# Performance work log

Measured on AMD Instinct MI355X. Metric: run time of the kernel, lower is better.

Reference implementation:

```python
import jax, jax.numpy as jnp
import numpy as np

K = 20
EPS = 1e-5   # BatchNorm eps (eval mode: running_mean=0, running_var=1)
SLOPE = 0.2


def knn_idx(x, k):
    # x: [B,F,N] -> idx [B,N,k]; top-k of negative squared distance (includes self)
    xx = jnp.sum(x * x, axis=1)                       # [B,N]
    inner = jnp.einsum('bfn,bfm->bnm', x, x)          # [B,N,N]
    neg_d = 2.0 * inner - xx[:, :, None] - xx[:, None, :]
    _, idx = jax.lax.top_k(neg_d, k)
    return idx


def gather_neighbors(x_nt, idx):
    # x_nt [B,N,F], idx [B,N,k] -> [B,N,k,F]
    return jax.vmap(lambda xt, ix: xt[ix])(x_nt, idx)


def group_layer(x_bfn, idx):
    # GroupLayer: [B,F,N] -> [B,2F,N,k] = cat(neigh - center, neigh)
    x_nt = jnp.transpose(x_bfn, (0, 2, 1))
    neigh = gather_neighbors(x_nt, idx)
    feat = jnp.concatenate([neigh - x_nt[:, :, None, :], neigh], axis=-1)
    return jnp.transpose(feat, (0, 3, 1, 2))


def eigen_graph(pts_bfn, k):
    # pts_bfn [B,3,N] -> feature [B,15,N], idx_EU [B,N,k], idx_EI [B,N,k]
    B, _, N = pts_bfn.shape
    idx_eu = knn_idx(pts_bfn, k)
    pts_nt = jnp.transpose(pts_bfn, (0, 2, 1))        # [B,N,3]
    neigh = gather_neighbors(pts_nt, idx_eu)          # [B,N,k,3]
    diff = neigh - pts_nt[:, :, None, :]
    cov = jnp.einsum('bnki,bnkj->bnij', diff, diff)   # [B,N,3,3] symmetric PSD
    eigval, eigvec = jnp.linalg.eigh(cov)             # [B,N,3], [B,N,3,3]
    feature = jnp.concatenate([pts_nt, eigval, eigvec.reshape(B, N, 9)], axis=2)
    idx_ei = knn_idx(jnp.transpose(eigval, (0, 2, 1)), k)
    return jnp.transpose(feature, (0, 2, 1)), idx_eu, idx_ei


def first_group_layer(x_bfn, idx_eu, idx_ei):
    # x_bfn [B,15,N]: [:,0:3]=xyz, [:,3:6]=eigenvalues -> [B,12,N,k]
    xyz = jnp.transpose(x_bfn[:, 0:3, :], (0, 2, 1))
    eig = jnp.transpose(x_bfn[:, 3:6, :], (0, 2, 1))
    nx = gather_neighbors(xyz, idx_eu)
    gx = jnp.concatenate([nx - xyz[:, :, None, :], nx], axis=-1)
    ne = gather_neighbors(eig, idx_ei)
    ge = jnp.concatenate([ne - eig[:, :, None, :], ne], axis=-1)
    out = jnp.concatenate([gx, ge], axis=-1)
    return jnp.transpose(out, (0, 3, 1, 2))


def graph_distance(pts_bfn, idx):
    pts_nt = jnp.transpose(pts_bfn, (0, 2, 1))
    d = gather_neighbors(pts_nt, idx) - pts_nt[:, :, None, :]
    s = jnp.sum(d * d, axis=-1)
    return jnp.sqrt(jnp.maximum(s, 1e-12))[:, None, :, :]  # [B,1,N,k]


def conv_bn_lrelu(x, w, g, b):
    # 1x1 conv (no bias) + eval-mode BN + LeakyReLU(0.2)
    if x.ndim == 4:
        y = jnp.einsum('oc,bcnk->bonk', w, x)
        g_, b_ = g[None, :, None, None], b[None, :, None, None]
    else:
        y = jnp.einsum('oc,bcn->bon', w, x)
        g_, b_ = g[None, :, None], b[None, :, None]
    y = y / jnp.sqrt(1.0 + EPS) * g_ + b_
    return jax.nn.leaky_relu(y, SLOPE)


def fps(points, n_samples):
    # furthest point sampling, start at index 0. points [B,N,3] -> [B,S] int32
    B, N, _ = points.shape
    init = jnp.zeros((B,), jnp.int32)
    dist0 = jnp.full((B, N), 1e10, points.dtype)

    def body(carry, _):
        dist, last = carry
        lastp = jnp.take_along_axis(points, last[:, None, None].astype(jnp.int32), axis=1)
        d = jnp.sum((points - lastp) ** 2, axis=-1)
        dist = jnp.minimum(dist, d)
        nxt = jnp.argmax(dist, axis=-1).astype(jnp.int32)
        return (dist, nxt), nxt

    (_, _), rest = jax.lax.scan(body, (dist0, init), None, length=n_samples - 1)
    return jnp.concatenate([init[None, :], rest], axis=0).T


def gather_op(x_bcn, idx):
    # x [B,C,N], idx [B,S] -> [B,C,S]
    return jnp.take_along_axis(x_bcn, idx[:, None, :], axis=2)


def forward(x, conv1_w, bn1_g, bn1_b, conv2_w, bn2_g, bn2_b, conv3_w, bn3_g, bn3_b,
            conv5_w, bn5_g, bn5_b, lin1_w, bn6_g, bn6_b, lin2_w, lin2_b,
            bn7_g, bn7_b, lin3_w, lin3_b):
    B, _, N1 = x.shape
    N2, N3 = N1 // 2, N1 // 4
    pts1 = jnp.transpose(x, (0, 2, 1))  # [B,N,3]

    # GSCM layer 1 (first layer)
    feat, idx_eu, idx_ei = eigen_graph(x, K)
    g = first_group_layer(feat, idx_eu, idx_ei)            # [B,12,N1,K]
    g = jnp.concatenate([g, graph_distance(x, idx_eu)], axis=1)  # [B,13,N1,K]
    x1 = conv_bn_lrelu(g, conv1_w, bn1_g, bn1_b).max(axis=-1)     # [B,64,N1]

    # downsample to N2
    id2 = fps(pts1, N2)
    pts2_bfn = gather_op(x, id2)                            # [B,3,N2]
    x1_ds = gather_op(x1, id2)                              # [B,64,N2]

    # GSCM layer 2
    _, idx_eu2, idx_ei2 = eigen_graph(pts2_bfn, K)
    g2 = jnp.concatenate([group_layer(x1_ds, idx_eu2), group_layer(x1_ds, idx_ei2)], axis=1)
    x2 = conv_bn_lrelu(g2, conv2_w, bn2_g, bn2_b).max(axis=-1)    # [B,64,N2]

    # downsample to N3
    pts2_nt = jnp.transpose(pts2_bfn, (0, 2, 1))
    id3 = fps(pts2_nt, N3)
    pts3_bfn = gather_op(pts2_bfn, id3)
    x2_ds = gather_op(x2, id3)
    x1_ds = gather_op(x1_ds, id3)

    # GSCM layer 3
    _, idx_eu3, idx_ei3 = eigen_graph(pts3_bfn, K)
    g3 = jnp.concatenate([group_layer(x2_ds, idx_eu3), group_layer(x2_ds, idx_ei3)], axis=1)
    x3 = conv_bn_lrelu(g3, conv3_w, bn3_g, bn3_b).max(axis=-1)    # [B,128,N3]

    h = jnp.concatenate([x1_ds, x2_ds, x3], axis=1)        # [B,256,N3]
    h = conv_bn_lrelu(h, conv5_w, bn5_g, bn5_b)            # [B,emb,N3]
    h = jnp.concatenate([h.max(axis=-1), h.mean(axis=-1)], axis=1)  # [B,2*emb]

    y = jnp.einsum('oi,bi->bo', lin1_w, h)
    y = jax.nn.leaky_relu(y / jnp.sqrt(1.0 + EPS) * bn6_g + bn6_b, SLOPE)
    y = jnp.einsum('oi,bi->bo', lin2_w, y) + lin2_b
    y = jax.nn.leaky_relu(y / jnp.sqrt(1.0 + EPS) * bn7_g + bn7_b, SLOPE)
    return jnp.einsum('oi,bi->bo', lin3_w, y) + lin3_b     # [B,40]


def setup_inputs() -> dict:
    key = jax.random.key(0)
    ks = jax.random.split(key, 10)
    B, N, EMB, OUT = 16, 1024, 1024, 40

    def w(k_, o, i):
        return jax.random.normal(k_, (o, i), jnp.float32) * (1.0 / np.sqrt(i))

    return {
        'x': jax.random.normal(ks[0], (B, 3, N), jnp.float32),
        'conv1_w': w(ks[1], 64, 13), 'bn1_g': jnp.ones((64,)), 'bn1_b': jnp.zeros((64,)),
        'conv2_w': w(ks[2], 64, 256), 'bn2_g': jnp.ones((64,)), 'bn2_b': jnp.zeros((64,)),
        'conv3_w': w(ks[3], 128, 256), 'bn3_g': jnp.ones((128,)), 'bn3_b': jnp.zeros((128,)),
        'conv5_w': w(ks[4], EMB, 256), 'bn5_g': jnp.ones((EMB,)), 'bn5_b': jnp.zeros((EMB,)),
        'lin1_w': w(ks[5], 512, 2 * EMB), 'bn6_g': jnp.ones((512,)), 'bn6_b': jnp.zeros((512,)),
        'lin2_w': w(ks[6], 256, 512), 'lin2_b': jnp.zeros((256,)),
        'bn7_g': jnp.ones((256,)), 'bn7_b': jnp.zeros((256,)),
        'lin3_w': w(ks[7], OUT, 256), 'lin3_b': jnp.zeros((OUT,)),
    }


def reference(x, conv1_w, bn1_g, bn1_b, conv2_w, bn2_g, bn2_b, conv3_w, bn3_g, bn3_b,
              conv5_w, bn5_g, bn5_b, lin1_w, bn6_g, bn6_b, lin2_w, lin2_b,
              bn7_g, bn7_b, lin3_w, lin3_b):
    return forward(x, conv1_w, bn1_g, bn1_b, conv2_w, bn2_g, bn2_b, conv3_w, bn3_g, bn3_b,
                   conv5_w, bn5_g, bn5_b, lin1_w, bn6_g, bn6_b, lin2_w, lin2_b,
                   bn7_g, bn7_b, lin3_w, lin3_b)
```

## Files before the change

kernel.cpp:

```cpp
#include <hip/hip_runtime.h>
#include <math.h>

#define KNB 20
constexpr float BN_INV = 0.9999950000374997f;
constexpr float SLOPE = 0.2f;

__device__ __forceinline__ float lrelu(float v){ return v >= 0.f ? v : SLOPE*v; }

__global__ __launch_bounds__(256) void prep_kernel(const float* __restrict__ x, float* __restrict__ pts,
                            const float* __restrict__ conv2w, float* __restrict__ Wc2,
                            const float* __restrict__ conv3w, float* __restrict__ Wc3){
  int i = blockIdx.x*256 + threadIdx.x;
  if (i < 16*1024){
    int b = i >> 10, n = i & 1023;
    const float* xb = x + (size_t)b*3*1024;
    float* p = pts + (size_t)i*3;
    p[0]=xb[n]; p[1]=xb[1024+n]; p[2]=xb[2048+n];
  } else if (i < 16*1024 + 64*64){
    int e = i - 16*1024;
    int o = e >> 6, c = e & 63;
    float wa=conv2w[(size_t)o*256+c], wb=conv2w[(size_t)o*256+64+c];
    float wc=conv2w[(size_t)o*256+128+c], wd=conv2w[(size_t)o*256+192+c];
    Wc2[((size_t)0*64+o)*64+c]=wa+wb; Wc2[((size_t)1*64+o)*64+c]=wc+wd; Wc2[((size_t)2*64+o)*64+c]=wa+wc;
  } else if (i < 16*1024 + 64*64 + 128*64){
    int e = i - 16*1024 - 64*64;
    int o = e >> 6, c = e & 63;
    float wa=conv3w[(size_t)o*256+c], wb=conv3w[(size_t)o*256+64+c];
    float wc=conv3w[(size_t)o*256+128+c], wd=conv3w[(size_t)o*256+192+c];
    Wc3[((size_t)0*128+o)*64+c]=wa+wb; Wc3[((size_t)1*128+o)*64+c]=wc+wd; Wc3[((size_t)2*128+o)*64+c]=wa+wc;
  }
}

template<int N, bool TOGLOBAL>
__device__ void knn_core(const float* __restrict__ pts, int* __restrict__ idx_global,
                         int* __restrict__ sOut, int chunk, int b, float4* sp){
#pragma clang fp contract(off)
  constexpr int E = N/64;
  int t = threadIdx.x;
  const float* pb = pts + (size_t)b*N*3;
  for (int e = t; e < N; e += 256){
    float x0=pb[e*3], x1=pb[e*3+1], x2=pb[e*3+2];
    sp[e] = make_float4(x0, x1, x2, (x0*x0 + x1*x1) + x2*x2);
  }
  __syncthreads();
  int wave = t >> 6, lane = t & 63;
  int row = chunk*4 + wave;
  float4 P = sp[row];
  float nd[E];
  #pragma unroll
  for (int i=0;i<E;++i){
    float4 Q = sp[lane + i*64];
    float inner = (P.x*Q.x + P.y*Q.y) + P.z*Q.z;
    nd[i] = (2.0f*inner - P.w) - Q.w;
  }
  int myout = 0;
  for (int j=0;j<KNB;++j){
    float bv = nd[0]; int bi = lane;
    #pragma unroll
    for (int i=1;i<E;++i){
      if (nd[i] > bv){ bv = nd[i]; bi = lane + i*64; }
    }
    #pragma unroll
    for (int off=1; off<64; off<<=1){
      float ov = __shfl_xor(bv, off);
      int oi = __shfl_xor(bi, off);
      if (ov > bv || (ov == bv && oi < bi)){ bv = ov; bi = oi; }
    }
    if (lane == j) myout = bi;
    if (lane == (bi & 63)){
      int slot = bi >> 6;
      #pragma unroll
      for (int i=0;i<E;++i) if (i == slot) nd[i] = -INFINITY;
    }
  }
  if (TOGLOBAL){
    if (lane < KNB) idx_global[((size_t)b*N + row)*KNB + lane] = myout;
  } else {
    if (lane < KNB) sOut[lane] = myout;
  }
}

template<int N>
__global__ __launch_bounds__(256) void knn_kernel(const float* __restrict__ pts, int* __restrict__ idx){
  __shared__ float4 sp[N];
  knn_core<N,true>(pts, idx, nullptr, blockIdx.x, blockIdx.y, sp);
}

#define DECLQ(i) float4 Q##i = sp[(i)*64+lane]; float D##i = 1e10f; \
  asm volatile("" : "+v"(Q##i.x), "+v"(Q##i.y), "+v"(Q##i.z));
#define UPD(i, B) { float dx=Q##i.x-L.x; float dy=Q##i.y-L.y; float dz=Q##i.z-L.z; \
  float dd=fminf(D##i,(dx*dx+dy*dy)+dz*dz); D##i=dd; \
  unsigned long long k=((unsigned long long)__float_as_uint(dd)<<32)|(unsigned long long)(nl-(unsigned)((i)*64)); \
  if(k>B)B=k; }
#define DPPMAX(ctrl) { unsigned lo=(unsigned)bk, hi=(unsigned)(bk>>32); \
  unsigned lo2=(unsigned)__builtin_amdgcn_mov_dpp((int)lo, ctrl, 0xF, 0xF, true); \
  unsigned hi2=(unsigned)__builtin_amdgcn_mov_dpp((int)hi, ctrl, 0xF, 0xF, true); \
  unsigned long long ok=((unsigned long long)hi2<<32)|lo2; if(ok>bk)bk=ok; }
#define FPS_TAIL \
      unsigned long long kl_ = b0>b1?b0:b1; unsigned long long kh_ = b2>b3?b2:b3; \
      unsigned long long bk = kl_>kh_?kl_:kh_; \
      DPPMAX(0xB1) DPPMAX(0x4E) DPPMAX(0x124) DPPMAX(0x128) \
      { unsigned long long ok=__shfl_xor(bk,16); if(ok>bk)bk=ok; } \
      { unsigned long long ok=__shfl_xor(bk,32); if(ok>bk)bk=ok; } \
      last = (int)(~(unsigned int)bk); \
      if (lane==0) idout[(size_t)b*M + s] = last;

template<int N, int M>
__device__ void fps_body(const float* __restrict__ pts, int* __restrict__ idout,
                         int b, float4* sp){
#pragma clang fp contract(off)
  constexpr int E = N/64;
  int tid = threadIdx.x;
  const float* pb = pts + (size_t)b*N*3;
  for (int e=tid; e<N; e+=256){
    sp[e] = make_float4(pb[e*3], pb[e*3+1], pb[e*3+2], 0.f);
  }
  __syncthreads();
  if (tid >= 64) return;
  __builtin_amdgcn_s_setprio(1);
  int lane = tid;
  unsigned int nl = ~(unsigned int)lane;
  int last = 0;
  if (lane==0) idout[(size_t)b*M] = 0;
  if constexpr (E == 16){
    DECLQ(0) DECLQ(1) DECLQ(2) DECLQ(3) DECLQ(4) DECLQ(5) DECLQ(6) DECLQ(7)
    DECLQ(8) DECLQ(9) DECLQ(10) DECLQ(11) DECLQ(12) DECLQ(13) DECLQ(14) DECLQ(15)
    for (int s=1; s<M; ++s){
      float4 L = sp[last];
      unsigned long long b0=0ULL,b1=0ULL,b2=0ULL,b3=0ULL;
      UPD(0,b0) UPD(1,b1) UPD(2,b2) UPD(3,b3)
      UPD(4,b0) UPD(5,b1) UPD(6,b2) UPD(7,b3)
      UPD(8,b0) UPD(9,b1) UPD(10,b2) UPD(11,b3)
      UPD(12,b0) UPD(13,b1) UPD(14,b2) UPD(15,b3)
      FPS_TAIL
    }
  } else {
    DECLQ(0) DECLQ(1) DECLQ(2) DECLQ(3) DECLQ(4) DECLQ(5) DECLQ(6) DECLQ(7)
    for (int s=1; s<M; ++s){
      float4 L = sp[last];
      unsigned long long b0=0ULL,b1=0ULL,b2=0ULL,b3=0ULL;
      UPD(0,b0) UPD(1,b1) UPD(2,b2) UPD(3,b3)
      UPD(4,b0) UPD(5,b1) UPD(6,b2) UPD(7,b3)
      FPS_TAIL
    }
  }
}

template<int N, int M>
__global__ __launch_bounds__(256, 1) void mega_knn_fps_kernel(const float* __restrict__ pts,
    int* __restrict__ knn_idx, int* __restrict__ fps_id){
  __shared__ float4 sp[N];
  if (blockIdx.x < 16){
    fps_body<N,M>(pts, fps_id, blockIdx.x, sp);
  } else {
    int bx = blockIdx.x - 16;
    knn_core<N,true>(pts, knn_idx, nullptr, bx % (N/4), bx / (N/4), sp);
  }
}

template<int N>
__global__ void cov_eig_kernel(const float* __restrict__ pts, const int* __restrict__ idx,
                               float* __restrict__ eigval){
  int i = blockIdx.x*blockDim.x + threadIdx.x;
  if (i >= 16*N) return;
  int b = i / N, n = i % N;
  const float* pb = pts + (size_t)b*N*3;
  const int* ix = idx + (size_t)i*KNB;
  float cx = pb[n*3], cy = pb[n*3+1], cz = pb[n*3+2];
  float c00=0,c01=0,c02=0,c11=0,c12=0,c22=0;
  for (int k=0;k<KNB;++k){
    int m = ix[k];
    float dx = pb[m*3]-cx, dy = pb[m*3+1]-cy, dz = pb[m*3+2]-cz;
    c00 += dx*dx; c01 += dx*dy; c02 += dx*dz;
    c11 += dy*dy; c12 += dy*dz; c22 += dz*dz;
  }
  double a00=c00,a01=c01,a02=c02,a11=c11,a12=c12,a22=c22;
  double p1 = a01*a01 + a02*a02 + a12*a12;
  double q = (a00+a11+a22)/3.0;
  double b00=a00-q, b11=a11-q, b22=a22-q;
  double p2 = b00*b00+b11*b11+b22*b22 + 2.0*p1;
  double e0,e1,e2;
  if (p2 <= 0.0){
    e0=e1=e2=q;
  } else {
    double p = sqrt(p2/6.0);
    double det = b00*(b11*b22 - a12*a12) - a01*(a01*b22 - a12*a02) + a02*(a01*a12 - b11*a02);
    double r = det / (2.0*p*p*p);
    r = fmin(1.0, fmax(-1.0, r));
    double phi = acos(r)/3.0;
    double big = q + 2.0*p*cos(phi);
    double sml = q + 2.0*p*cos(phi + 2.0943951023931953);
    double mid = 3.0*q - big - sml;
    e0 = sml; e1 = mid; e2 = big;
  }
  float* ev = eigval + (size_t)i*3;
  ev[0]=(float)e0; ev[1]=(float)e1; ev[2]=(float)e2;
}

__global__ __launch_bounds__(256) void knn_ei_stage1_kernel(
    const float* __restrict__ eig, const float* __restrict__ pts,
    const int* __restrict__ idx_eu,
    const float* __restrict__ w, const float* __restrict__ g, const float* __restrict__ bb,
    float* __restrict__ x1){
  constexpr int N = 1024;
  __shared__ float4 sp[N];
  __shared__ int sIei[4][KNB];
  __shared__ float feat[4][13][KNB];
  int b = blockIdx.y, chunk = blockIdx.x;
  int t = threadIdx.x, wave = t>>6, lane = t&63;
  knn_core<N,false>(eig, nullptr, &sIei[wave][0], chunk, b, sp);
  int row = chunk*4 + wave;
  size_t i = (size_t)b*N + row;
  const float* pb = pts + (size_t)b*N*3;
  if (lane < KNB){
    int ieu = idx_eu[i*KNB + lane];
    int iei = sIei[wave][lane];
    float4 ne4 = sp[iei];
    float4 ee4 = sp[row];
    float d2 = 0.f;
    #pragma unroll
    for (int f=0; f<3; ++f){
      float nx = pb[ieu*3+f], xx = pb[row*3+f];
      float dfv = nx - xx;
      feat[wave][f][lane] = dfv; feat[wave][3+f][lane] = nx;
      float ne = (f==0)? ne4.x : ((f==1)? ne4.y : ne4.z);
      float ee = (f==0)? ee4.x : ((f==1)? ee4.y : ee4.z);
      feat[wave][6+f][lane] = ne - ee; feat[wave][9+f][lane] = ne;
      d2 += dfv*dfv;
    }
    feat[wave][12][lane] = sqrtf(fmaxf(d2, 1e-12f));
  }
  __syncthreads();
  float wr[13];
  #pragma unroll
  for (int c=0;c<13;++c) wr[c] = w[lane*13+c];
  float sg = BN_INV * g[lane], sb = bb[lane];
  float mx = -INFINITY;
  for (int k=0;k<KNB;++k){
    float s = 0.f;
    #pragma unroll
    for (int c=0;c<13;++c) s = fmaf(wr[c], feat[wave][c][k], s);
    mx = fmaxf(mx, lrelu(fmaf(s, sg, sb)));
  }
  x1[i*64 + lane] = mx;
}

template<int COUT, int N>
__device__ void gm_body(const float* __restrict__ eig,
    const float* __restrict__ PQR, int Mtot,
    const int* __restrict__ idx_eu,
    const float* __restrict__ g, const float* __restrict__ bb,
    float* __restrict__ xout, int chunk, int b, float4* sp, int* sIeiW){
  int t = threadIdx.x, wave = t>>6, lane = t&63;
  knn_core<N,false>(eig, nullptr, sIeiW, chunk, b, sp);
  __syncthreads();
  int row = chunk*4 + wave;
  size_t i = (size_t)b*N + row;
  const float* P = PQR;
  const float* Q = PQR + (size_t)Mtot*COUT;
  const float* R = PQR + (size_t)2*Mtot*COUT;
  for (int o = lane; o < COUT; o += 64){
    float base = R[i*COUT + o];
    float sg = BN_INV*g[o], sb = bb[o];
    float mx = -INFINITY;
    for (int k=0;k<KNB;++k){
      int eu = idx_eu[i*KNB + k];
      int ei = sIeiW[k];
      float v = P[((size_t)b*N + eu)*COUT + o] + Q[((size_t)b*N + ei)*COUT + o] - base;
      mx = fmaxf(mx, lrelu(fmaf(v, sg, sb)));
    }
    xout[i*COUT + o] = mx;
  }
}

template<int COUT, int N>
__global__ __launch_bounds__(256) void knn_ei_gm_kernel(
    const float* __restrict__ eig, const float* __restrict__ PQR, int Mtot,
    const int* __restrict__ idx_eu, const float* __restrict__ g, const float* __restrict__ bb,
    float* __restrict__ xout){
  __shared__ float4 sp[N];
  __shared__ int sIei[4][KNB];
  int wave = threadIdx.x >> 6;
  gm_body<COUT,N>(eig, PQR, Mtot, idx_eu, g, bb, xout, blockIdx.x, blockIdx.y, sp, &sIei[wave][0]);
}

template<int COUT, int N, int M>
__global__ __launch_bounds__(256, 1) void gmfps_kernel(
    const float* __restrict__ eig, const float* __restrict__ ptsN,
    const float* __restrict__ PQR, int Mtot,
    const int* __restrict__ idx_eu, const float* __restrict__ g, const float* __restrict__ bb,
    float* __restrict__ xout, int* __restrict__ fps_id){
  __shared__ float4 sp[N];
  __shared__ int sIei[4][KNB];
  if (blockIdx.x < 16){
    fps_body<N,M>(ptsN, fps_id, blockIdx.x, sp);
    return;
  }
  int bx = blockIdx.x - 16;
  int wave = threadIdx.x >> 6;
  gm_body<COUT,N>(eig, PQR, Mtot, idx_eu, g, bb, xout, bx % (N/4), bx / (N/4), sp, &sIei[wave][0]);
}

__global__ __launch_bounds__(256) void gather2_kernel(const float* __restrict__ pts1, const float* __restrict__ x1,
                               const int* __restrict__ id2, float* __restrict__ pts2, float* __restrict__ x1d){
  int i = blockIdx.x*256 + threadIdx.x;
  if (i < 16*512){
    int b = i >> 9;
    int src = id2[i];
    const float* p = pts1 + ((size_t)b*1024 + src)*3;
    float* o = pts2 + (size_t)i*3;
    o[0]=p[0]; o[1]=p[1]; o[2]=p[2];
  } else {
    int e = i - 16*512;
    if (e < 16*512*64){
      int c = e & 63, r = e >> 6;
      int b = r >> 9, s = r & 511;
      int src = id2[(size_t)b*512 + s];
      x1d[e] = x1[((size_t)b*1024 + src)*64 + c];
    }
  }
}

__global__ __launch_bounds__(256) void gather3_kernel(const float* __restrict__ pts2, const float* __restrict__ x2,
                               const float* __restrict__ x1d, const int* __restrict__ id3,
                               float* __restrict__ pts3, float* __restrict__ x2d, float* __restrict__ x1dd){
  int i = blockIdx.x*256 + threadIdx.x;
  if (i < 16*256){
    int b = i >> 8;
    int src = id3[i];
    const float* p = pts2 + ((size_t)b*512 + src)*3;
    float* o = pts3 + (size_t)i*3;
    o[0]=p[0]; o[1]=p[1]; o[2]=p[2];
  } else {
    int e = i - 16*256;
    if (e < 16*256*64){
      int c = e & 63, r = e >> 6;
      int b = r >> 8, s = r & 255;
      int src = id3[(size_t)b*256 + s];
      x2d[e] = x2[((size_t)b*512 + src)*64 + c];
    } else {
      int e2 = e - 16*256*64;
      if (e2 < 16*256*64){
        int c = e2 & 63, r = e2 >> 6;
        int b = r >> 8, s = r & 255;
        int src = id3[(size_t)b*256 + s];
        x1dd[e2] = x1d[((size_t)b*512 + src)*64 + c];
      }
    }
  }
}

template<int COUT>
__global__ __launch_bounds__(256) void gemm_xw_kernel(
    const float* __restrict__ X, const float* __restrict__ Wc,
    float* __restrict__ PQR, int Mtot){
  __shared__ float sA[64][68];
  __shared__ float sW[64][68];
  int mt = blockIdx.x, ot = blockIdx.y, set = blockIdx.z;
  int t = threadIdx.x;
  for (int e=t; e<4096; e+=256){ int r=e>>6, c=e&63; sA[r][c] = X[(size_t)(mt*64+r)*64 + c]; }
  const float* Wp = Wc + ((size_t)set*COUT + ot*64)*64;
  for (int e=t; e<4096; e+=256){ int r=e>>6, c=e&63; sW[r][c] = Wp[(size_t)r*64 + c]; }
  __syncthreads();
  int tx = t & 15, ty = t >> 4;
  float acc[4][4];
  #pragma unroll
  for (int r=0;r<4;++r)
    #pragma unroll
    for (int j=0;j<4;++j) acc[r][j]=0.f;
  #pragma unroll
  for (int k4=0;k4<16;++k4){
    float4 A0 = *(const float4*)&sA[ty*4+0][k4*4];
    float4 A1 = *(const float4*)&sA[ty*4+1][k4*4];
    float4 A2 = *(const float4*)&sA[ty*4+2][k4*4];
    float4 A3 = *(const float4*)&sA[ty*4+3][k4*4];
    float4 W0 = *(const float4*)&sW[tx*4+0][k4*4];
    float4 W1 = *(const float4*)&sW[tx*4+1][k4*4];
    float4 W2 = *(const float4*)&sW[tx*4+2][k4*4];
    float4 W3 = *(const float4*)&sW[tx*4+3][k4*4];
    float4 A[4] = {A0,A1,A2,A3};
    float4 W[4] = {W0,W1,W2,W3};
    #pragma unroll
    for (int r=0;r<4;++r)
      #pragma unroll
      for (int j=0;j<4;++j){
        float s = acc[r][j];
        s = fmaf(A[r].x, W[j].x, s);
        s = fmaf(A[r].y, W[j].y, s);
        s = fmaf(A[r].z, W[j].z, s);
        s = fmaf(A[r].w, W[j].w, s);
        acc[r][j] = s;
      }
  }
  float* outp = PQR + (size_t)set*Mtot*COUT;
  #pragma unroll
  for (int r=0;r<4;++r){
    float4 v = make_float4(acc[r][0], acc[r][1], acc[r][2], acc[r][3]);
    *(float4*)&outp[(size_t)(mt*64 + ty*4 + r)*COUT + ot*64 + tx*4] = v;
  }
}

__global__ __launch_bounds__(256) void conv5_gemm_kernel(
    const float* __restrict__ x1dd, const float* __restrict__ x2d, const float* __restrict__ x3,
    const float* __restrict__ w, const float* __restrict__ g, const float* __restrict__ bb,
    float* __restrict__ pmax, float* __restrict__ psum){
  __shared__ float sA[64][68];
  __shared__ float sB[64][68];
  int otile = blockIdx.x, ntile = blockIdx.y, b = blockIdx.z;
  int t = threadIdx.x;
  int tx = t & 15, ty = t >> 4;
  float acc[4][4];
  #pragma unroll
  for (int i=0;i<4;++i)
    #pragma unroll
    for (int j=0;j<4;++j) acc[i][j] = 0.f;
  for (int kc=0; kc<4; ++kc){
    #pragma unroll 4
    for (int e = t; e < 4096; e += 256){
      int nl = e >> 6, kl = e & 63;
      int n = ntile*64 + nl;
      float v;
      if (kc == 0)      v = x1dd[((size_t)b*256 + n)*64 + kl];
      else if (kc == 1) v = x2d [((size_t)b*256 + n)*64 + kl];
      else              v = x3  [((size_t)b*256 + n)*128 + (kc-2)*64 + kl];
      sA[nl][kl] = v;
    }
    #pragma unroll 4
    for (int e = t; e < 4096; e += 256){
      int ol = e >> 6, kl = e & 63;
      sB[ol][kl] = w[((size_t)(otile*64 + ol))*256 + kc*64 + kl];
    }
    __syncthreads();
    #pragma unroll
    for (int k4=0; k4<16; ++k4){
      float4 a0 = *(const float4*)&sA[ty*4+0][k4*4];
      float4 a1 = *(const float4*)&sA[ty*4+1][k4*4];
      float4 a2 = *(const float4*)&sA[ty*4+2][k4*4];
      float4 a3 = *(const float4*)&sA[ty*4+3][k4*4];
      float4 b0 = *(const float4*)&sB[tx*4+0][k4*4];
      float4 b1 = *(const float4*)&sB[tx*4+1][k4*4];
      float4 b2 = *(const float4*)&sB[tx*4+2][k4*4];
      float4 b3 = *(const float4*)&sB[tx*4+3][k4*4];
      float4 A[4] = {a0,a1,a2,a3};
      float4 Bv[4] = {b0,b1,b2,b3};
      #pragma unroll
      for (int i=0;i<4;++i)
        #pragma unroll
        for (int j=0;j<4;++j){
          float s = acc[i][j];
          s = fmaf(A[i].x, Bv[j].x, s);
          s = fmaf(A[i].y, Bv[j].y, s);
          s = fmaf(A[i].z, Bv[j].z, s);
          s = fmaf(A[i].w, Bv[j].w, s);
          acc[i][j] = s;
        }
    }
    __syncthreads();
  }
  float sg[4], sbv[4];
  #pragma unroll
  for (int j=0;j<4;++j){
    int o = otile*64 + tx*4 + j;
    sg[j] = BN_INV*g[o]; sbv[j] = bb[o];
  }
  float mx[4], sm[4];
  #pragma unroll
  for (int j=0;j<4;++j){ mx[j]=-INFINITY; sm[j]=0.f; }
  #pragma unroll
  for (int i=0;i<4;++i)
    #pragma unroll
    for (int j=0;j<4;++j){
      float vv = lrelu(fmaf(acc[i][j], sg[j], sbv[j]));
      mx[j] = fmaxf(mx[j], vv);
      sm[j] += vv;
    }
  float* redM = &sA[0][0];
  float* redS = redM + 16*64;
  #pragma unroll
  for (int j=0;j<4;++j){
    redM[ty*64 + tx*4 + j] = mx[j];
    redS[ty*64 + tx*4 + j] = sm[j];
  }
  __syncthreads();
  if (t < 64){
    float m = -INFINITY, s = 0.f;
    #pragma unroll
    for (int r=0;r<16;++r){
      m = fmaxf(m, redM[r*64 + t]);
      s += redS[r*64 + t];
    }
    int o = otile*64 + t;
    pmax[((size_t)b*1024 + o)*4 + ntile] = m;
    psum[((size_t)b*1024 + o)*4 + ntile] = s;
  }
}

__global__ void head_reduce_kernel(const float* __restrict__ pmax, const float* __restrict__ psum,
                                   float* __restrict__ h2){
  int i = blockIdx.x*blockDim.x + threadIdx.x;
  if (i >= 16*1024) return;
  int b = i >> 10, o = i & 1023;
  const float* pm = pmax + (size_t)i*4;
  const float* ps = psum + (size_t)i*4;
  float mx = fmaxf(fmaxf(pm[0],pm[1]), fmaxf(pm[2],pm[3]));
  float sm = (ps[0]+ps[1])+(ps[2]+ps[3]);
  h2[(size_t)b*2048 + o] = mx;
  h2[(size_t)b*2048 + 1024 + o] = sm * (1.0f/256.0f);
}

__global__ __launch_bounds__(256) void lin1_kernel(const float* __restrict__ h2, const float* __restrict__ w,
    const float* __restrict__ g, const float* __restrict__ bb, float* __restrict__ y1){
  __shared__ float sh[2048];
  int b = blockIdx.y; int o = blockIdx.x*256 + threadIdx.x;
  for (int e=threadIdx.x; e<2048; e+=256) sh[e] = h2[(size_t)b*2048+e];
  __syncthreads();
  const float* wr = w + (size_t)o*2048;
  float acc=0.f;
  for (int c=0;c<2048;++c) acc = fmaf(wr[c], sh[c], acc);
  y1[(size_t)b*512+o] = lrelu(fmaf(acc, BN_INV*g[o], bb[o]));
}

__global__ __launch_bounds__(256) void lin2_kernel(const float* __restrict__ y1, const float* __restrict__ w,
    const float* __restrict__ lb, const float* __restrict__ g, const float* __restrict__ bb,
    float* __restrict__ y2){
  __shared__ float sh[512];
  int b = blockIdx.x; int o = threadIdx.x;
  for (int e=o; e<512; e+=256) sh[e]=y1[(size_t)b*512+e];
  __syncthreads();
  const float* wr = w + (size_t)o*512;
  float acc=0.f;
  for (int c=0;c<512;++c) acc = fmaf(wr[c], sh[c], acc);
  acc += lb[o];
  y2[(size_t)b*256+o] = lrelu(fmaf(acc, BN_INV*g[o], bb[o]));
}

__global__ __launch_bounds__(64) void lin3_kernel(const float* __restrict__ y2, const float* __restrict__ w,
    const float* __restrict__ lb, float* __restrict__ outp){
  __shared__ float sh[256];
  int b = blockIdx.x; int t = threadIdx.x;
  for (int e=t; e<256; e+=64) sh[e]=y2[(size_t)b*256+e];
  __syncthreads();
  if (t < 40){
    const float* wr = w + (size_t)t*256;
    float acc=0.f;
    for (int c=0;c<256;++c) acc = fmaf(wr[c], sh[c], acc);
    outp[(size_t)b*40+t] = acc + lb[t];
  }
}

extern "C" void kernel_launch(void* const* d_in, const int* in_sizes, int n_in,
                              void* d_out, int out_size, void* d_ws, size_t ws_size,
                              hipStream_t stream) {
  const float* x      = (const float*)d_in[0];
  const float* conv1w = (const float*)d_in[1];
  const float* bn1g   = (const float*)d_in[2];
  const float* bn1b   = (const float*)d_in[3];
  const float* conv2w = (const float*)d_in[4];
  const float* bn2g   = (const float*)d_in[5];
  const float* bn2b   = (const float*)d_in[6];
  const float* conv3w = (const float*)d_in[7];
  const float* bn3g   = (const float*)d_in[8];
  const float* bn3b   = (const float*)d_in[9];
  const float* conv5w = (const float*)d_in[10];
  const float* bn5g   = (const float*)d_in[11];
  const float* bn5b   = (const float*)d_in[12];
  const float* lin1w  = (const float*)d_in[13];
  const float* bn6g   = (const float*)d_in[14];
  const float* bn6b   = (const float*)d_in[15];
  const float* lin2w  = (const float*)d_in[16];
  const float* lin2b  = (const float*)d_in[17];
  const float* bn7g   = (const float*)d_in[18];
  const float* bn7b   = (const float*)d_in[19];
  const float* lin3w  = (const float*)d_in[20];
  const float* lin3b  = (const float*)d_in[21];
  float* outp = (float*)d_out;

  char* ws = (char*)d_ws;
  size_t off = 0;
  auto alloc = [&](size_t bytes)->char*{
    off = (off + 255) & ~(size_t)255;
    char* p = ws + off; off += bytes; return p;
  };
  const int B=16, N1=1024, N2=512, N3=256;
  float* pts1 = (float*)alloc((size_t)B*N1*3*4);
  int*   ieu1 = (int*)alloc((size_t)B*N1*KNB*4);
  float* eig1 = (float*)alloc((size_t)B*N1*3*4);
  float* x1   = (float*)alloc((size_t)B*N1*64*4);
  int*   id2  = (int*)alloc((size_t)B*N2*4);
  float* pts2 = (float*)alloc((size_t)B*N2*3*4);
  float* x1d  = (float*)alloc((size_t)B*N2*64*4);
  int*   ieu2 = (int*)alloc((size_t)B*N2*KNB*4);
  float* eig2 = (float*)alloc((size_t)B*N2*3*4);
  float* x2   = (float*)alloc((size_t)B*N2*64*4);
  int*   id3  = (int*)alloc((size_t)B*N3*4);
  float* pts3 = (float*)alloc((size_t)B*N3*3*4);
  float* x2d  = (float*)alloc((size_t)B*N3*64*4);
  float* x1dd = (float*)alloc((size_t)B*N3*64*4);
  int*   ieu3 = (int*)alloc((size_t)B*N3*KNB*4);
  float* eig3 = (float*)alloc((size_t)B*N3*3*4);
  float* x3   = (float*)alloc((size_t)B*N3*128*4);
  float* pmax = (float*)alloc((size_t)B*1024*4*4);
  float* psum = (float*)alloc((size_t)B*1024*4*4);
  float* h2   = (float*)alloc((size_t)B*2048*4);
  float* y1   = (float*)alloc((size_t)B*512*4);
  float* y2   = (float*)alloc((size_t)B*256*4);
  float* Wc2  = (float*)alloc((size_t)3*64*64*4);
  float* Wc3  = (float*)alloc((size_t)3*128*64*4);
  float* PQR2 = (float*)alloc((size_t)3*B*N2*64*4);
  float* PQR3 = (float*)alloc((size_t)3*B*N3*128*4);

  prep_kernel<<<112, 256, 0, stream>>>(x, pts1, conv2w, Wc2, conv3w, Wc3);
  mega_knn_fps_kernel<1024,512><<<16 + 4096, 256, 0, stream>>>(pts1, ieu1, id2);
  cov_eig_kernel<1024><<<(B*N1+255)/256, 256, 0, stream>>>(pts1, ieu1, eig1);
  knn_ei_stage1_kernel<<<dim3(256,16), 256, 0, stream>>>(eig1, pts1, ieu1, conv1w, bn1g, bn1b, x1);
  gather2_kernel<<<2080, 256, 0, stream>>>(pts1, x1, id2, pts2, x1d);
  knn_kernel<512><<<dim3(128,16), 256, 0, stream>>>(pts2, ieu2);
  gemm_xw_kernel<64><<<dim3(B*N2/64, 1, 3), 256, 0, stream>>>(x1d, Wc2, PQR2, B*N2);
  cov_eig_kernel<512><<<(B*N2+255)/256, 256, 0, stream>>>(pts2, ieu2, eig2);
  gmfps_kernel<64,512,256><<<16 + 2048, 256, 0, stream>>>(eig2, pts2, PQR2, B*N2, ieu2, bn2g, bn2b, x2, id3);
  gather3_kernel<<<2064, 256, 0, stream>>>(pts2, x2, x1d, id3, pts3, x2d, x1dd);
  knn_kernel<256><<<dim3(64,16), 256, 0, stream>>>(pts3, ieu3);
  cov_eig_kernel<256><<<(B*N3+255)/256, 256, 0, stream>>>(pts3, ieu3, eig3);
  gemm_xw_kernel<128><<<dim3(B*N3/64, 2, 3), 256, 0, stream>>>(x2d, Wc3, PQR3, B*N3);
  knn_ei_gm_kernel<128,256><<<dim3(64,16), 256, 0, stream>>>(eig3, PQR3, B*N3, ieu3, bn3g, bn3b, x3);
  conv5_gemm_kernel<<<dim3(16,4,16), 256, 0, stream>>>(x1dd, x2d, x3, conv5w, bn5g, bn5b, pmax, psum);
  head_reduce_kernel<<<(B*1024+255)/256, 256, 0, stream>>>(pmax, psum, h2);
  lin1_kernel<<<dim3(2,16), 256, 0, stream>>>(h2, lin1w, bn6g, bn6b, y1);
  lin2_kernel<<<16, 256, 0, stream>>>(y1, lin2w, lin2b, bn7g, bn7b, y2);
  lin3_kernel<<<16, 64, 0, stream>>>(y2, lin3w, lin3b, outp);
}
```

Before: 707.0 us.

## Spread FPS over four waves and fuse head reduce and linear kernels

Farthest point sampling now uses all four waves of its block instead of one. Each thread holds fewer points, and each iteration ends with a cross-wave argmax through a double-buffered shared array plus a block barrier. The head reduction is folded into lin1's shared-memory load, and lin2 and lin3 are merged into one kernel, which removes two launches and two intermediate buffers. The FPS change swaps a shorter per-wave serial chain for a __syncthreads on each of its 511 or 255 sequential steps.

```diff
diff --git a/kernel.cpp b/kernel.cpp
--- a/kernel.cpp
+++ b/kernel.cpp
@@ -86,62 +86,63 @@
   knn_core<N,true>(pts, idx, nullptr, blockIdx.x, blockIdx.y, sp);
 }
 
-#define DECLQ(i) float4 Q##i = sp[(i)*64+lane]; float D##i = 1e10f; \
+#define DECLQ4(i) float4 Q##i = sp[(i)*256 + tid]; float D##i = 1e10f; \
   asm volatile("" : "+v"(Q##i.x), "+v"(Q##i.y), "+v"(Q##i.z));
-#define UPD(i, B) { float dx=Q##i.x-L.x; float dy=Q##i.y-L.y; float dz=Q##i.z-L.z; \
+#define UPD4(i, B) { float dx=Q##i.x-L.x; float dy=Q##i.y-L.y; float dz=Q##i.z-L.z; \
   float dd=fminf(D##i,(dx*dx+dy*dy)+dz*dz); D##i=dd; \
-  unsigned long long k=((unsigned long long)__float_as_uint(dd)<<32)|(unsigned long long)(nl-(unsigned)((i)*64)); \
+  unsigned long long k=((unsigned long long)__float_as_uint(dd)<<32)|(unsigned long long)(nl-(unsigned)((i)*256)); \
   if(k>B)B=k; }
 #define DPPMAX(ctrl) { unsigned lo=(unsigned)bk, hi=(unsigned)(bk>>32); \
   unsigned lo2=(unsigned)__builtin_amdgcn_mov_dpp((int)lo, ctrl, 0xF, 0xF, true); \
   unsigned hi2=(unsigned)__builtin_amdgcn_mov_dpp((int)hi, ctrl, 0xF, 0xF, true); \
   unsigned long long ok=((unsigned long long)hi2<<32)|lo2; if(ok>bk)bk=ok; }
-#define FPS_TAIL \
-      unsigned long long kl_ = b0>b1?b0:b1; unsigned long long kh_ = b2>b3?b2:b3; \
-      unsigned long long bk = kl_>kh_?kl_:kh_; \
+#define FPS_STEP_TAIL \
       DPPMAX(0xB1) DPPMAX(0x4E) DPPMAX(0x124) DPPMAX(0x128) \
       { unsigned long long ok=__shfl_xor(bk,16); if(ok>bk)bk=ok; } \
       { unsigned long long ok=__shfl_xor(bk,32); if(ok>bk)bk=ok; } \
-      last = (int)(~(unsigned int)bk); \
-      if (lane==0) idout[(size_t)b*M + s] = last;
+      if (lane==0) rk[((s&1)<<2) | w] = bk; \
+      __syncthreads(); \
+      const unsigned long long* rp = rk + ((s&1)<<2); \
+      unsigned long long k0=rp[0], k1=rp[1], k2=rp[2], k3=rp[3]; \
+      unsigned long long km1 = k0>k1?k0:k1, km2 = k2>k3?k2:k3; \
+      unsigned long long kk = km1>km2?km1:km2; \
+      last = (int)(~(unsigned int)kk); \
+      if (tid==0) idout[(size_t)b*M + s] = last;
 
 template<int N, int M>
-__device__ void fps_body(const float* __restrict__ pts, int* __restrict__ idout,
-                         int b, float4* sp){
+__device__ void fps_body4(const float* __restrict__ pts, int* __restrict__ idout,
+                          int b, float4* sp, unsigned long long* rk){
 #pragma clang fp contract(off)
-  constexpr int E = N/64;
+  constexpr int E4 = N/256;
   int tid = threadIdx.x;
   const float* pb = pts + (size_t)b*N*3;
   for (int e=tid; e<N; e+=256){
     sp[e] = make_float4(pb[e*3], pb[e*3+1], pb[e*3+2], 0.f);
   }
   __syncthreads();
-  if (tid >= 64) return;
   __builtin_amdgcn_s_setprio(1);
-  int lane = tid;
-  unsigned int nl = ~(unsigned int)lane;
+  int lane = tid & 63, w = tid >> 6;
+  unsigned int nl = ~(unsigned int)tid;
   int last = 0;
-  if (lane==0) idout[(size_t)b*M] = 0;
-  if constexpr (E == 16){
-    DECLQ(0) DECLQ(1) DECLQ(2) DECLQ(3) DECLQ(4) DECLQ(5) DECLQ(6) DECLQ(7)
-    DECLQ(8) DECLQ(9) DECLQ(10) DECLQ(11) DECLQ(12) DECLQ(13) DECLQ(14) DECLQ(15)
+  if (tid==0) idout[(size_t)b*M] = 0;
+  if constexpr (E4 == 4){
+    DECLQ4(0) DECLQ4(1) DECLQ4(2) DECLQ4(3)
     for (int s=1; s<M; ++s){
       float4 L = sp[last];
       unsigned long long b0=0ULL,b1=0ULL,b2=0ULL,b3=0ULL;
-      UPD(0,b0) UPD(1,b1) UPD(2,b2) UPD(3,b3)
-      UPD(4,b0) UPD(5,b1) UPD(6,b2) UPD(7,b3)
-      UPD(8,b0) UPD(9,b1) UPD(10,b2) UPD(11,b3)
-      UPD(12,b0) UPD(13,b1) UPD(14,b2) UPD(15,b3)
-      FPS_TAIL
+      UPD4(0,b0) UPD4(1,b1) UPD4(2,b2) UPD4(3,b3)
+      unsigned long long kl_ = b0>b1?b0:b1, kh_ = b2>b3?b2:b3;
+      unsigned long long bk = kl_>kh_?kl_:kh_;
+      FPS_STEP_TAIL
     }
   } else {
-    DECLQ(0) DECLQ(1) DECLQ(2) DECLQ(3) DECLQ(4) DECLQ(5) DECLQ(6) DECLQ(7)
+    DECLQ4(0) DECLQ4(1)
     for (int s=1; s<M; ++s){
       float4 L = sp[last];
-      unsigned long long b0=0ULL,b1=0ULL,b2=0ULL,b3=0ULL;
-      UPD(0,b0) UPD(1,b1) UPD(2,b2) UPD(3,b3)
-      UPD(4,b0) UPD(5,b1) UPD(6,b2) UPD(7,b3)
-      FPS_TAIL
+      unsigned long long b0=0ULL,b1=0ULL;
+      UPD4(0,b0) UPD4(1,b1)
+      unsigned long long bk = b0>b1?b0:b1;
+      FPS_STEP_TAIL
     }
   }
 }
@@ -150,8 +151,9 @@
 __global__ __launch_bounds__(256, 1) void mega_knn_fps_kernel(const float* __restrict__ pts,
     int* __restrict__ knn_idx, int* __restrict__ fps_id){
   __shared__ float4 sp[N];
+  __shared__ unsigned long long rk[8];
   if (blockIdx.x < 16){
-    fps_body<N,M>(pts, fps_id, blockIdx.x, sp);
+    fps_body4<N,M>(pts, fps_id, blockIdx.x, sp, rk);
   } else {
     int bx = blockIdx.x - 16;
     knn_core<N,true>(pts, knn_idx, nullptr, bx % (N/4), bx / (N/4), sp);
@@ -292,8 +294,9 @@
     float* __restrict__ xout, int* __restrict__ fps_id){
   __shared__ float4 sp[N];
   __shared__ int sIei[4][KNB];
+  __shared__ unsigned long long rk[8];
   if (blockIdx.x < 16){
-    fps_body<N,M>(ptsN, fps_id, blockIdx.x, sp);
+    fps_body4<N,M>(ptsN, fps_id, blockIdx.x, sp, rk);
     return;
   }
   int bx = blockIdx.x - 16;
@@ -495,24 +498,20 @@
   }
 }
 
-__global__ void head_reduce_kernel(const float* __restrict__ pmax, const float* __restrict__ psum,
-                                   float* __restrict__ h2){
-  int i = blockIdx.x*blockDim.x + threadIdx.x;
-  if (i >= 16*1024) return;
-  int b = i >> 10, o = i & 1023;
-  const float* pm = pmax + (size_t)i*4;
-  const float* ps = psum + (size_t)i*4;
-  float mx = fmaxf(fmaxf(pm[0],pm[1]), fmaxf(pm[2],pm[3]));
-  float sm = (ps[0]+ps[1])+(ps[2]+ps[3]);
-  h2[(size_t)b*2048 + o] = mx;
-  h2[(size_t)b*2048 + 1024 + o] = sm * (1.0f/256.0f);
-}
-
-__global__ __launch_bounds__(256) void lin1_kernel(const float* __restrict__ h2, const float* __restrict__ w,
-    const float* __restrict__ g, const float* __restrict__ bb, float* __restrict__ y1){
+__global__ __launch_bounds__(256) void lin1_kernel(const float* __restrict__ pmax, const float* __restrict__ psum,
+    const float* __restrict__ w, const float* __restrict__ g, const float* __restrict__ bb,
+    float* __restrict__ y1){
   __shared__ float sh[2048];
   int b = blockIdx.y; int o = blockIdx.x*256 + threadIdx.x;
-  for (int e=threadIdx.x; e<2048; e+=256) sh[e] = h2[(size_t)b*2048+e];
+  for (int e=threadIdx.x; e<2048; e+=256){
+    if (e < 1024){
+      const float* pm = pmax + ((size_t)b*1024 + e)*4;
+      sh[e] = fmaxf(fmaxf(pm[0],pm[1]), fmaxf(pm[2],pm[3]));
+    } else {
+      const float* ps = psum + ((size_t)b*1024 + (e-1024))*4;
+      sh[e] = ((ps[0]+ps[1])+(ps[2]+ps[3])) * (1.0f/256.0f);
+    }
+  }
   __syncthreads();
   const float* wr = w + (size_t)o*2048;
   float acc=0.f;
@@ -520,31 +519,29 @@
   y1[(size_t)b*512+o] = lrelu(fmaf(acc, BN_INV*g[o], bb[o]));
 }
 
-__global__ __launch_bounds__(256) void lin2_kernel(const float* __restrict__ y1, const float* __restrict__ w,
-    const float* __restrict__ lb, const float* __restrict__ g, const float* __restrict__ bb,
-    float* __restrict__ y2){
-  __shared__ float sh[512];
+__global__ __launch_bounds__(256) void lin23_kernel(const float* __restrict__ y1,
+    const float* __restrict__ w2, const float* __restrict__ lb2,
+    const float* __restrict__ g, const float* __restrict__ bb,
+    const float* __restrict__ w3, const float* __restrict__ lb3,
+    float* __restrict__ outp){
+  __shared__ float sh1[512];
+  __shared__ float sh2[256];
   int b = blockIdx.x; int o = threadIdx.x;
-  for (int e=o; e<512; e+=256) sh[e]=y1[(size_t)b*512+e];
-  __syncthreads();
-  const float* wr = w + (size_t)o*512;
-  float acc=0.f;
-  for (int c=0;c<512;++c) acc = fmaf(wr[c], sh[c], acc);
-  acc += lb[o];
-  y2[(size_t)b*256+o] = lrelu(fmaf(acc, BN_INV*g[o], bb[o]));
-}
-
-__global__ __launch_bounds__(64) void lin3_kernel(const float* __restrict__ y2, const float* __restrict__ w,
-    const float* __restrict__ lb, float* __restrict__ outp){
-  __shared__ float sh[256];
-  int b = blockIdx.x; int t = threadIdx.x;
-  for (int e=t; e<256; e+=64) sh[e]=y2[(size_t)b*256+e];
-  __syncthreads();
-  if (t < 40){
-    const float* wr = w + (size_t)t*256;
+  for (int e=o; e<512; e+=256) sh1[e]=y1[(size_t)b*512+e];
+  __syncthreads();
+  {
+    const float* wr = w2 + (size_t)o*512;
     float acc=0.f;
-    for (int c=0;c<256;++c) acc = fmaf(wr[c], sh[c], acc);
-    outp[(size_t)b*40+t] = acc + lb[t];
+    for (int c=0;c<512;++c) acc = fmaf(wr[c], sh1[c], acc);
+    acc += lb2[o];
+    sh2[o] = lrelu(fmaf(acc, BN_INV*g[o], bb[o]));
+  }
+  __syncthreads();
+  if (o < 40){
+    const float* wr = w3 + (size_t)o*256;
+    float acc=0.f;
+    for (int c=0;c<256;++c) acc = fmaf(wr[c], sh2[c], acc);
+    outp[(size_t)b*40+o] = acc + lb3[o];
   }
 }
 
@@ -601,9 +598,7 @@
   float* x3   = (float*)alloc((size_t)B*N3*128*4);
   float* pmax = (float*)alloc((size_t)B*1024*4*4);
   float* psum = (float*)alloc((size_t)B*1024*4*4);
-  float* h2   = (float*)alloc((size_t)B*2048*4);
   float* y1   = (float*)alloc((size_t)B*512*4);
-  float* y2   = (float*)alloc((size_t)B*256*4);
   float* Wc2  = (float*)alloc((size_t)3*64*64*4);
   float* Wc3  = (float*)alloc((size_t)3*128*64*4);
   float* PQR2 = (float*)alloc((size_t)3*B*N2*64*4);
@@ -624,8 +619,6 @@
   gemm_xw_kernel<128><<<dim3(B*N3/64, 2, 3), 256, 0, stream>>>(x2d, Wc3, PQR3, B*N3);
   knn_ei_gm_kernel<128,256><<<dim3(64,16), 256, 0, stream>>>(eig3, PQR3, B*N3, ieu3, bn3g, bn3b, x3);
   conv5_gemm_kernel<<<dim3(16,4,16), 256, 0, stream>>>(x1dd, x2d, x3, conv5w, bn5g, bn5b, pmax, psum);
-  head_reduce_kernel<<<(B*1024+255)/256, 256, 0, stream>>>(pmax, psum, h2);
-  lin1_kernel<<<dim3(2,16), 256, 0, stream>>>(h2, lin1w, bn6g, bn6b, y1);
-  lin2_kernel<<<16, 256, 0, stream>>>(y1, lin2w, lin2b, bn7g, bn7b, y2);
-  lin3_kernel<<<16, 64, 0, stream>>>(y2, lin3w, lin3b, outp);
-}
+  lin1_kernel<<<dim3(2,16), 256, 0, stream>>>(pmax, psum, lin1w, bn6g, bn6b, y1);
+  lin23_kernel<<<16, 256, 0, stream>>>(y1, lin2w, lin2b, bn7g, bn7b, lin3w, lin3b, outp);
+}
```

Result: faster. 660.8 us (-6.5%).
